# Kernel optimization log

Hardware: AMD Instinct MI355X
Metric: run time of the kernel (lower is better)

Reference implementation:

```python
import jax, jax.numpy as jnp
import numpy as np

N, E, IN, HID, H, OUT = 50000, 1600000, 64, 128, 4, 64
D = HID // H  # per-head dim = 32
EPS = 1e-5
NEG_SLOPE = 0.2


def layer_norm(x, g, b):
    mu = x.mean(-1, keepdims=True)
    var = ((x - mu) ** 2).mean(-1, keepdims=True)
    return (x - mu) * jax.lax.rsqrt(var + EPS) * g + b


def gat_conv(h, src, dst, W, a_src, a_dst, bias):
    # h: [N, HID]; W: [HID, H*D]; a_src/a_dst: [H, D]
    hW = (h @ W).reshape(N, H, D)
    e_src = (hW * a_src).sum(-1)  # [N, H]
    e_dst = (hW * a_dst).sum(-1)  # [N, H]
    e = jax.nn.leaky_relu(e_src[src] + e_dst[dst], NEG_SLOPE)  # [Etot, H]
    m = jax.ops.segment_max(e, dst, num_segments=N)            # [N, H]
    ex = jnp.exp(e - m[dst])
    denom = jax.ops.segment_sum(ex, dst, num_segments=N)       # [N, H]
    alpha = ex / denom[dst]                                    # [Etot, H]
    out = jax.ops.segment_sum(alpha[:, :, None] * hW[src], dst, num_segments=N)
    return out.reshape(N, H * D) + bias


def setup_inputs():
    key = jax.random.key(0)
    ks = jax.random.split(key, 16)
    s = 0.05
    return {
        "x": jax.random.normal(ks[0], (N, IN), jnp.float32),
        "edge_index": jax.random.randint(ks[1], (2, E), 0, N, jnp.int64),
        "w_in": jax.random.normal(ks[2], (IN, HID), jnp.float32) * s,
        "b_in": jnp.zeros((HID,), jnp.float32),
        "g1": jnp.ones((HID,), jnp.float32),
        "be1": jnp.zeros((HID,), jnp.float32),
        "W1": jax.random.normal(ks[3], (HID, H * D), jnp.float32) * s,
        "as1": jax.random.normal(ks[4], (H, D), jnp.float32) * s,
        "ad1": jax.random.normal(ks[5], (H, D), jnp.float32) * s,
        "bg1": jnp.zeros((H * D,), jnp.float32),
        "g2": jnp.ones((HID,), jnp.float32),
        "be2": jnp.zeros((HID,), jnp.float32),
        "W2": jax.random.normal(ks[6], (HID, H * D), jnp.float32) * s,
        "as2": jax.random.normal(ks[7], (H, D), jnp.float32) * s,
        "ad2": jax.random.normal(ks[8], (H, D), jnp.float32) * s,
        "bg2": jnp.zeros((H * D,), jnp.float32),
        "w_out": jax.random.normal(ks[9], (HID, OUT), jnp.float32) * s,
        "b_out": jnp.zeros((OUT,), jnp.float32),
    }


def reference(x, edge_index, w_in, b_in, g1, be1, W1, as1, ad1, bg1,
              g2, be2, W2, as2, ad2, bg2, w_out, b_out):
    # PyG GATConv default add_self_loops=True
    loops = jnp.arange(N, dtype=edge_index.dtype)
    src = jnp.concatenate([edge_index[0], loops])
    dst = jnp.concatenate([edge_index[1], loops])

    h = x @ w_in + b_in
    h = jax.nn.gelu(layer_norm(h, g1, be1))
    h = gat_conv(h, src, dst, W1, as1, ad1, bg1)
    h = jax.nn.gelu(layer_norm(h, g2, be2))
    # dropout: identity in eval mode
    h = gat_conv(h, src, dst, W2, as2, ad2, bg2)
    return h @ w_out + b_out
```

## Files before the change

kernel.cpp:

```cpp
#include <hip/hip_runtime.h>
#include <hip/hip_bf16.h>
#include <math.h>

#define NN   50000
#define EE   1600000
#define ETOT (EE + NN)
#define HID  128
#define INF_ 64
#define OUTF 64

#define NBK  256
#define NPB  196
#define CAP  8192
#define BBLK 256
#define CHUNK ((ETOT + BBLK - 1) / BBLK)

#define PADX 72
#define PADH 136

typedef short  short8  __attribute__((ext_vector_type(8)));
typedef float  floatx4 __attribute__((ext_vector_type(4)));
typedef float  floatx2 __attribute__((ext_vector_type(2)));

__device__ __forceinline__ ushort f2b(float f) {
    __hip_bfloat16 h = __float2bfloat16(f);
    return *reinterpret_cast<ushort*>(&h);
}

__device__ __forceinline__ float gelu_f(float x) {
    float x2 = x * x;
    float u  = 0.7978845608f * fmaf(0.044715f * x2, x, x);
    u = fminf(u, 40.f);
    float t = __expf(2.f * u);
    return x * t / (t + 1.f);
}


__global__ __launch_bounds__(1024) void k_bucket(const int* __restrict__ ei,
                                                 int* bcur, int* __restrict__ tmp) {
    __shared__ unsigned sortedv[CHUNK];
    __shared__ int hist[NBK], gbase[NBK], loff[NBK], lcur[NBK];
    int t = threadIdx.x;
    int lo = blockIdx.x * CHUNK;
    int hi = min(lo + CHUNK, ETOT);
    int bsize = hi - lo;
    if (t < NBK) hist[t] = 0;
    __syncthreads();
    for (int i = lo + t; i < hi; i += 1024) {
        int d = (i < EE) ? ei[EE + i] : i - EE;
        atomicAdd(&hist[d / NPB], 1);
    }
    __syncthreads();
    if (t < NBK) {
        int c = hist[t];
        gbase[t] = (c > 0) ? atomicAdd(&bcur[t], c) : 0;
        loff[t] = c;
    }
    __syncthreads();
    for (int d = 1; d < NBK; d <<= 1) {
        int v = (t >= d && t < NBK) ? loff[t - d] : 0;
        __syncthreads();
        if (t < NBK) loff[t] += v;
        __syncthreads();
    }
    if (t < NBK) {
        int ex = loff[t] - hist[t];
        loff[t] = ex;
        lcur[t] = ex;
    }
    __syncthreads();
    for (int i = lo + t; i < hi; i += 1024) {
        unsigned s, d;
        if (i < EE) { s = (unsigned)ei[i]; d = (unsigned)ei[EE + i]; }
        else        { s = d = (unsigned)(i - EE); }
        unsigned b = d / NPB;
        int p = atomicAdd(&lcur[b], 1);
        sortedv[p] = (b << 24) | (s << 8) | (d - b * NPB);
    }
    __syncthreads();
    for (int i = t; i < bsize; i += 1024) {
        unsigned v = sortedv[i];
        unsigned b = v >> 24;
        int pp = gbase[b] + i - loff[b];
        if (pp < CAP) tmp[b * CAP + pp] = (int)(v & 0xFFFFFFu);
    }
}

__global__ __launch_bounds__(256) void k_bscan(const int* __restrict__ bcur,
                                               int* __restrict__ bstart,
                                               int* __restrict__ off,
                                               int* __restrict__ csr) {
    __shared__ int s[NBK];
    int t = threadIdx.x;
    int v0 = bcur[t];
    s[t] = v0;
    __syncthreads();
    for (int d = 1; d < NBK; d <<= 1) {
        int v = (t >= d) ? s[t - d] : 0;
        __syncthreads();
        s[t] += v;
        __syncthreads();
    }
    bstart[t] = s[t] - v0;
    if (t == 0) off[NN] = ETOT;
    if (t < 64) csr[ETOT + t] = 0;
}

__global__ __launch_bounds__(512) void k_bucket2csr(const int* __restrict__ tmp,
                                                    const int* __restrict__ bcur,
                                                    const int* __restrict__ bstart,
                                                    int* __restrict__ off,
                                                    int* __restrict__ csr) {
    __shared__ int sE[CAP];
    __shared__ int lcnt[NPB];
    __shared__ int loff[NPB];
    int b = blockIdx.x, t = threadIdx.x;
    int n0    = b * NPB;
    int bsize = min(bcur[b], CAP);
    int base  = bstart[b];
    if (t < NPB) lcnt[t] = 0;
    for (int i = t; i < bsize; i += 512) sE[i] = tmp[b * CAP + i];
    __syncthreads();
    for (int i = t; i < bsize; i += 512) atomicAdd(&lcnt[sE[i] & 255], 1);
    __syncthreads();
    if (t < NPB) loff[t] = lcnt[t];
    __syncthreads();
    for (int d = 1; d < NPB; d <<= 1) {
        int v = (t >= d && t < NPB) ? loff[t - d] : 0;
        __syncthreads();
        if (t < NPB) loff[t] += v;
        __syncthreads();
    }
    if (t < NPB) {
        int ex = loff[t] - lcnt[t];
        if (n0 + t < NN) off[n0 + t] = base + ex;
        lcnt[t] = ex;
    }
    __syncthreads();
    for (int i = t; i < bsize; i += 512) {
        int v   = sE[i];
        int pos = base + atomicAdd(&lcnt[v & 255], 1);
        csr[pos] = v >> 8;
    }
}


__global__ void k_packall(const float* __restrict__ w_in, const float* __restrict__ W1,
                          const float* __restrict__ W2, ushort* __restrict__ Bp1,
                          ushort* __restrict__ BpW1, ushort* __restrict__ BpW2,
                          int* __restrict__ bcur) {
    int tid = blockIdx.x * 256 + threadIdx.x;
    if (tid < NBK) bcur[tid] = 0;
    const float* W; ushort* dst; int K, id;
    if (tid < 1024)      { W = w_in; dst = Bp1;  K = 64;  id = tid; }
    else if (tid < 3072) { W = W1;   dst = BpW1; K = 128; id = tid - 1024; }
    else if (tid < 5120) { W = W2;   dst = BpW2; K = 128; id = tid - 3072; }
    else return;
    int kst = K >> 5;
    int l = id & 63;
    int s = (id >> 6) % kst;
    int T = id / (kst * 64);
    int m = l & 15, q = l >> 4;
    ushort o[8];
    #pragma unroll
    for (int j = 0; j < 8; ++j)
        o[j] = f2b(W[(s * 32 + q * 8 + j) * 128 + T * 16 + m]);
    uint4 pk;
    pk.x = (unsigned)o[0] | ((unsigned)o[1] << 16);
    pk.y = (unsigned)o[2] | ((unsigned)o[3] << 16);
    pk.z = (unsigned)o[4] | ((unsigned)o[5] << 16);
    pk.w = (unsigned)o[6] | ((unsigned)o[7] << 16);
    reinterpret_cast<uint4*>(dst)[id] = pk;
}


__device__ __forceinline__ void pack_store_fp8(ushort* hbfw, int l, int n0w, bool active,
                                               uint* __restrict__ hW8) {
    if (!active) return;
    int row = l >> 2, ch = l & 3;
    uint ov[8];
    #pragma unroll
    for (int u = 0; u < 8; ++u) {
        int c0 = ch * 32 + u * 4;
        float f0 = __uint_as_float((uint)hbfw[row * PADH + c0 + 0] << 16);
        float f1 = __uint_as_float((uint)hbfw[row * PADH + c0 + 1] << 16);
        float f2 = __uint_as_float((uint)hbfw[row * PADH + c0 + 2] << 16);
        float f3 = __uint_as_float((uint)hbfw[row * PADH + c0 + 3] << 16);
        int pk = __builtin_amdgcn_cvt_pk_fp8_f32(f0, f1, 0, false);
        pk     = __builtin_amdgcn_cvt_pk_fp8_f32(f2, f3, pk, true);
        ov[u] = (uint)pk;
    }
    uint4* dst = reinterpret_cast<uint4*>(hW8 + (size_t)(n0w + row) * 32 + ch * 8);
    dst[0] = make_uint4(ov[0], ov[1], ov[2], ov[3]);
    dst[1] = make_uint4(ov[4], ov[5], ov[6], ov[7]);
}


__global__ __launch_bounds__(128) void k_infeat(const float* __restrict__ x,
                                                const ushort* __restrict__ Bp1,
                                                const float* __restrict__ bin,
                                                const float* __restrict__ g,
                                                const float* __restrict__ be,
                                                const ushort* __restrict__ Bp2,
                                                const float* __restrict__ asrc,
                                                const float* __restrict__ adst,
                                                uint* __restrict__ hW8,
                                                float* __restrict__ esrc,
                                                float* __restrict__ edst) {
    __shared__ ushort xbf[2][16 * PADX];
    __shared__ ushort hbf[2][16 * PADH];
    int t = threadIdx.x, w = t >> 6, l = t & 63;
    int m = l & 15, q = l >> 4;
    int n0w = blockIdx.x * 32 + w * 16;
    bool active = (n0w < NN);
    int nb = active ? n0w : 0;

    const float4* x4 = reinterpret_cast<const float4*>(x) + (size_t)nb * 16;
    #pragma unroll
    for (int i = 0; i < 4; ++i) {
        int f4 = l + 64 * i;
        int node = f4 >> 4, c4 = f4 & 15;
        float4 v = x4[f4];
        ushort4 pk = { f2b(v.x), f2b(v.y), f2b(v.z), f2b(v.w) };
        *reinterpret_cast<ushort4*>(&xbf[w][node * PADX + c4 * 4]) = pk;
    }
    __syncthreads();

    const short8* B1 = reinterpret_cast<const short8*>(Bp1);
    floatx4 acc1[8];
    #pragma unroll
    for (int T = 0; T < 8; ++T) acc1[T] = (floatx4){0.f, 0.f, 0.f, 0.f};
    #pragma unroll
    for (int s = 0; s < 2; ++s) {
        short8 a = *reinterpret_cast<const short8*>(&xbf[w][m * PADX + s * 32 + q * 8]);
        #pragma unroll
        for (int T = 0; T < 8; ++T) {
            short8 b = B1[(T * 2 + s) * 64 + l];
            acc1[T] = __builtin_amdgcn_mfma_f32_16x16x32_bf16(a, b, acc1[T], 0, 0, 0);
        }
    }

    float bc[8], gc[8], bec[8];
    #pragma unroll
    for (int T = 0; T < 8; ++T) {
        int c = T * 16 + m;
        bc[T] = bin[c]; gc[T] = g[c]; bec[T] = be[c];
    }
    #pragma unroll
    for (int j = 0; j < 4; ++j) {
        float s1 = 0.f, s2 = 0.f;
        #pragma unroll
        for (int T = 0; T < 8; ++T) {
            float v = acc1[T][j] + bc[T];
            s1 += v; s2 = fmaf(v, v, s2);
        }
        #pragma unroll
        for (int mk = 1; mk < 16; mk <<= 1) {
            s1 += __shfl_xor(s1, mk, 64);
            s2 += __shfl_xor(s2, mk, 64);
        }
        float mu = s1 * (1.f / 128.f);
        float var = s2 * (1.f / 128.f) - mu * mu;
        float rs = rsqrtf(var + 1e-5f);
        #pragma unroll
        for (int T = 0; T < 8; ++T) {
            float v = acc1[T][j] + bc[T];
            float y = (v - mu) * rs * gc[T] + bec[T];
            hbf[w][(q * 4 + j) * PADH + T * 16 + m] = f2b(gelu_f(y));
        }
    }
    __syncthreads();

    const short8* B2 = reinterpret_cast<const short8*>(Bp2);
    floatx4 acc2[8];
    #pragma unroll
    for (int T = 0; T < 8; ++T) acc2[T] = (floatx4){0.f, 0.f, 0.f, 0.f};
    #pragma unroll
    for (int s = 0; s < 4; ++s) {
        short8 a = *reinterpret_cast<const short8*>(&hbf[w][m * PADH + s * 32 + q * 8]);
        #pragma unroll
        for (int T = 0; T < 8; ++T) {
            short8 b = B2[(T * 4 + s) * 64 + l];
            acc2[T] = __builtin_amdgcn_mfma_f32_16x16x32_bf16(a, b, acc2[T], 0, 0, 0);
        }
    }

    __syncthreads();
    #pragma unroll
    for (int j = 0; j < 4; ++j)
        #pragma unroll
        for (int T = 0; T < 8; ++T)
            hbf[w][(q * 4 + j) * PADH + T * 16 + m] = f2b(acc2[T][j]);
    __syncthreads();
    pack_store_fp8(hbf[w], l, n0w, active, hW8);

    float as_[8], ad_[8];
    #pragma unroll
    for (int T = 0; T < 8; ++T) {
        int c = T * 16 + m;
        as_[T] = asrc[c]; ad_[T] = adst[c];
    }
    #pragma unroll
    for (int j = 0; j < 4; ++j) {
        #pragma unroll
        for (int h = 0; h < 4; ++h) {
            float v1 = fmaf(acc2[2 * h][j], as_[2 * h], acc2[2 * h + 1][j] * as_[2 * h + 1]);
            float v2 = fmaf(acc2[2 * h][j], ad_[2 * h], acc2[2 * h + 1][j] * ad_[2 * h + 1]);
            #pragma unroll
            for (int mk = 1; mk < 16; mk <<= 1) {
                v1 += __shfl_xor(v1, mk, 64);
                v2 += __shfl_xor(v2, mk, 64);
            }
            if (m == 0 && active) {
                esrc[(n0w + q * 4 + j) * 4 + h] = v1;
                edst[(n0w + q * 4 + j) * 4 + h] = v2;
            }
        }
    }
}


__global__ __launch_bounds__(128) void k_feat(const float* __restrict__ hin,
                                              const float* __restrict__ g,
                                              const float* __restrict__ be,
                                              const ushort* __restrict__ Bp2,
                                              const float* __restrict__ asrc,
                                              const float* __restrict__ adst,
                                              uint* __restrict__ hW8,
                                              float* __restrict__ esrc,
                                              float* __restrict__ edst) {
    __shared__ ushort hbf[2][16 * PADH];
    int t = threadIdx.x, w = t >> 6, l = t & 63;
    int m = l & 15, q = l >> 4;
    int n0w = blockIdx.x * 32 + w * 16;
    bool active = (n0w < NN);
    int nb = active ? n0w : 0;

    const float4* h4g = reinterpret_cast<const float4*>(hin) + (size_t)nb * 32;
    const float4* g4  = reinterpret_cast<const float4*>(g);
    const float4* be4 = reinterpret_cast<const float4*>(be);
    #pragma unroll
    for (int i = 0; i < 8; ++i) {
        int f4 = l + 64 * i;
        int node = f4 >> 5, c4 = f4 & 31;
        float4 v = h4g[f4];
        float s1 = v.x + v.y + v.z + v.w;
        float s2 = fmaf(v.x, v.x, fmaf(v.y, v.y, fmaf(v.z, v.z, v.w * v.w)));
        #pragma unroll
        for (int mk = 1; mk < 32; mk <<= 1) {
            s1 += __shfl_xor(s1, mk, 64);
            s2 += __shfl_xor(s2, mk, 64);
        }
        float mu = s1 * (1.f / 128.f);
        float var = s2 * (1.f / 128.f) - mu * mu;
        float rs = rsqrtf(var + 1e-5f);
        float4 gg = g4[c4], bb = be4[c4];
        ushort4 pk;
        pk.x = f2b(gelu_f((v.x - mu) * rs * gg.x + bb.x));
        pk.y = f2b(gelu_f((v.y - mu) * rs * gg.y + bb.y));
        pk.z = f2b(gelu_f((v.z - mu) * rs * gg.z + bb.z));
        pk.w = f2b(gelu_f((v.w - mu) * rs * gg.w + bb.w));
        *reinterpret_cast<ushort4*>(&hbf[w][node * PADH + c4 * 4]) = pk;
    }
    __syncthreads();

    const short8* B2 = reinterpret_cast<const short8*>(Bp2);
    floatx4 acc2[8];
    #pragma unroll
    for (int T = 0; T < 8; ++T) acc2[T] = (floatx4){0.f, 0.f, 0.f, 0.f};
    #pragma unroll
    for (int s = 0; s < 4; ++s) {
        short8 a = *reinterpret_cast<const short8*>(&hbf[w][m * PADH + s * 32 + q * 8]);
        #pragma unroll
        for (int T = 0; T < 8; ++T) {
            short8 b = B2[(T * 4 + s) * 64 + l];
            acc2[T] = __builtin_amdgcn_mfma_f32_16x16x32_bf16(a, b, acc2[T], 0, 0, 0);
        }
    }

    __syncthreads();
    #pragma unroll
    for (int j = 0; j < 4; ++j)
        #pragma unroll
        for (int T = 0; T < 8; ++T)
            hbf[w][(q * 4 + j) * PADH + T * 16 + m] = f2b(acc2[T][j]);
    __syncthreads();
    pack_store_fp8(hbf[w], l, n0w, active, hW8);

    float as_[8], ad_[8];
    #pragma unroll
    for (int T = 0; T < 8; ++T) {
        int c = T * 16 + m;
        as_[T] = asrc[c]; ad_[T] = adst[c];
    }
    #pragma unroll
    for (int j = 0; j < 4; ++j) {
        #pragma unroll
        for (int h = 0; h < 4; ++h) {
            float v1 = fmaf(acc2[2 * h][j], as_[2 * h], acc2[2 * h + 1][j] * as_[2 * h + 1]);
            float v2 = fmaf(acc2[2 * h][j], ad_[2 * h], acc2[2 * h + 1][j] * ad_[2 * h + 1]);
            #pragma unroll
            for (int mk = 1; mk < 16; mk <<= 1) {
                v1 += __shfl_xor(v1, mk, 64);
                v2 += __shfl_xor(v2, mk, 64);
            }
            if (m == 0 && active) {
                esrc[(n0w + q * 4 + j) * 4 + h] = v1;
                edst[(n0w + q * 4 + j) * 4 + h] = v2;
            }
        }
    }
}


__global__ __launch_bounds__(128) void k_gat(const uint* __restrict__ hW8,
                                             const float* __restrict__ esrc,
                                             const float* __restrict__ edst,
                                             const int* __restrict__ off,
                                             const int* __restrict__ csr,
                                             const float* __restrict__ bg,
                                             float* __restrict__ out) {
    __shared__ float redA[16][8];
    __shared__ float redD[16];
    int n = blockIdx.x, t = threadIdx.x;
    int wv = t >> 6, l = t & 63;
    int slot = l >> 4;
    int q    = l & 15;
    int hq   = q >> 2;
    int o0 = off[n], o1 = off[n + 1];
    float ednh = edst[n * 4 + hq];
    const uint2* hw2 = reinterpret_cast<const uint2*>(hW8);
    floatx2 a01 = {0.f, 0.f}, a23 = {0.f, 0.f}, a45 = {0.f, 0.f}, a67 = {0.f, 0.f};
    float dsum = 0.f;
    int nIter = (o1 - o0 + 15) >> 4;
    int e = o0 + wv * 4 + slot;

    int srcA = csr[e];
    int srcB = csr[e + 8];
    int srcC = csr[e + 16];
    int srcD = csr[e + 24];
    float esA = esrc[srcA * 4 + hq];
    float esB = esrc[srcB * 4 + hq];
    uint2 rA = hw2[(size_t)srcA * 16 + q];
    uint2 rB = hw2[(size_t)srcB * 16 + q];

    for (int it = 0; it < nIter; ++it) {
        uint2 rC = hw2[(size_t)srcC * 16 + q];
        uint2 rD = hw2[(size_t)srcD * 16 + q];
        float esC = esrc[srcC * 4 + hq];
        float esD = esrc[srcD * 4 + hq];
        int srcE = csr[e + 32];
        int srcF = csr[e + 40];
        float ea = esA + ednh; ea = fmaxf(ea, 0.2f * ea);
        float eb = esB + ednh; eb = fmaxf(eb, 0.2f * eb);
        float wa = (e     < o1) ? __expf(ea) : 0.f;
        float wb = (e + 8 < o1) ? __expf(eb) : 0.f;
        floatx2 wa2 = {wa, wa}, wb2 = {wb, wb};
        a01 += wa2 * __builtin_amdgcn_cvt_pk_f32_fp8(rA.x, false);
        a23 += wa2 * __builtin_amdgcn_cvt_pk_f32_fp8(rA.x, true);
        a45 += wa2 * __builtin_amdgcn_cvt_pk_f32_fp8(rA.y, false);
        a67 += wa2 * __builtin_amdgcn_cvt_pk_f32_fp8(rA.y, true);
        a01 += wb2 * __builtin_amdgcn_cvt_pk_f32_fp8(rB.x, false);
        a23 += wb2 * __builtin_amdgcn_cvt_pk_f32_fp8(rB.x, true);
        a45 += wb2 * __builtin_amdgcn_cvt_pk_f32_fp8(rB.y, false);
        a67 += wb2 * __builtin_amdgcn_cvt_pk_f32_fp8(rB.y, true);
        dsum += wa + wb;
        e += 16;
        rA = rC; rB = rD;
        esA = esC; esB = esD;
        srcC = srcE; srcD = srcF;
    }
    float acc[8] = {a01[0], a01[1], a23[0], a23[1], a45[0], a45[1], a67[0], a67[1]};
    #pragma unroll
    for (int mk = 16; mk <= 32; mk <<= 1) {
        #pragma unroll
        for (int j = 0; j < 8; ++j) acc[j] += __shfl_xor(acc[j], mk, 64);
        dsum += __shfl_xor(dsum, mk, 64);
    }
    if (wv == 1 && l < 16) {
        #pragma unroll
        for (int j = 0; j < 8; ++j) redA[l][j] = acc[j];
        redD[l] = dsum;
    }
    __syncthreads();
    if (wv == 0 && l < 16) {
        float inv = 1.0f / (dsum + redD[l]);
        float4 r0, r1;
        r0.x = (acc[0] + redA[l][0]) * inv + bg[l * 8 + 0];
        r0.y = (acc[1] + redA[l][1]) * inv + bg[l * 8 + 1];
        r0.z = (acc[2] + redA[l][2]) * inv + bg[l * 8 + 2];
        r0.w = (acc[3] + redA[l][3]) * inv + bg[l * 8 + 3];
        r1.x = (acc[4] + redA[l][4]) * inv + bg[l * 8 + 4];
        r1.y = (acc[5] + redA[l][5]) * inv + bg[l * 8 + 5];
        r1.z = (acc[6] + redA[l][6]) * inv + bg[l * 8 + 6];
        r1.w = (acc[7] + redA[l][7]) * inv + bg[l * 8 + 7];
        float4* op = reinterpret_cast<float4*>(out + (size_t)n * HID + l * 8);
        op[0] = r0; op[1] = r1;
    }
}


__global__ __launch_bounds__(128) void k_out(const float* __restrict__ h,
                                             const float* __restrict__ w,
                                             const float* __restrict__ b,
                                             float* __restrict__ out) {
    __shared__ __align__(16) float hr[32 * 132];
    int t = threadIdx.x, n0 = blockIdx.x * 32;
    const float4* h4g = reinterpret_cast<const float4*>(h) + (size_t)n0 * 32;
    float4* hr4 = reinterpret_cast<float4*>(hr);
    #pragma unroll
    for (int i = 0; i < 8; ++i) {
        int f4 = t + 128 * i;
        hr4[(f4 >> 5) * 33 + (f4 & 31)] = h4g[f4];
    }
    __syncthreads();
    int cg = t & 15, ng = t >> 4;
    const float4* w4 = reinterpret_cast<const float4*>(w);
    float4 bb = reinterpret_cast<const float4*>(b)[cg];
    float4 acc[4] = {bb, bb, bb, bb};
    for (int k4 = 0; k4 < 32; ++k4) {
        float4 w0 = w4[(k4 * 4 + 0) * 16 + cg];
        float4 w1 = w4[(k4 * 4 + 1) * 16 + cg];
        float4 w2 = w4[(k4 * 4 + 2) * 16 + cg];
        float4 w3 = w4[(k4 * 4 + 3) * 16 + cg];
        #pragma unroll
        for (int r = 0; r < 4; ++r) {
            float4 hv = hr4[(ng * 4 + r) * 33 + k4];
            acc[r].x = fmaf(hv.x, w0.x, fmaf(hv.y, w1.x, fmaf(hv.z, w2.x, fmaf(hv.w, w3.x, acc[r].x))));
            acc[r].y = fmaf(hv.x, w0.y, fmaf(hv.y, w1.y, fmaf(hv.z, w2.y, fmaf(hv.w, w3.y, acc[r].y))));
            acc[r].z = fmaf(hv.x, w0.z, fmaf(hv.y, w1.z, fmaf(hv.z, w2.z, fmaf(hv.w, w3.z, acc[r].z))));
            acc[r].w = fmaf(hv.x, w0.w, fmaf(hv.y, w1.w, fmaf(hv.z, w2.w, fmaf(hv.w, w3.w, acc[r].w))));
        }
    }
    float4* o4 = reinterpret_cast<float4*>(out) + (size_t)n0 * 16;
    #pragma unroll
    for (int r = 0; r < 4; ++r) {
        if (n0 + ng * 4 + r < NN)
            o4[(ng * 4 + r) * 16 + cg] = acc[r];
    }
}

extern "C" void kernel_launch(void* const* d_in, const int* in_sizes, int n_in,
                              void* d_out, int out_size, void* d_ws, size_t ws_size,
                              hipStream_t stream) {
    const float* x    = (const float*)d_in[0];
    const int*   ei   = (const int*)  d_in[1];
    const float* w_in = (const float*)d_in[2];
    const float* b_in = (const float*)d_in[3];
    const float* g1   = (const float*)d_in[4];
    const float* be1  = (const float*)d_in[5];
    const float* W1   = (const float*)d_in[6];
    const float* as1  = (const float*)d_in[7];
    const float* ad1  = (const float*)d_in[8];
    const float* bg1  = (const float*)d_in[9];
    const float* g2   = (const float*)d_in[10];
    const float* be2  = (const float*)d_in[11];
    const float* W2   = (const float*)d_in[12];
    const float* as2  = (const float*)d_in[13];
    const float* ad2  = (const float*)d_in[14];
    const float* bg2  = (const float*)d_in[15];
    const float* w_o  = (const float*)d_in[16];
    const float* b_o  = (const float*)d_in[17];
    float* out = (float*)d_out;

    char* p = (char*)d_ws;
    auto take = [&](size_t bytes) {
        void* r = p;
        p += (bytes + 255) & ~(size_t)255;
        return r;
    };
    float*  gout  = (float*)take((size_t)NN * HID * 4);
    float*  h2    = (float*)take((size_t)NN * HID * 4);
    uint*   hW8   = (uint*)take((size_t)NN * HID);
    float*  esrc  = (float*)take((size_t)NN * 4 * 4);
    float*  edst  = (float*)take((size_t)NN * 4 * 4);
    int*    off   = (int*)take((size_t)(NN + 1) * 4);
    int*    csr   = (int*)take((size_t)(ETOT + 64) * 4);
    int*    tmp   = (int*)take((size_t)NBK * CAP * 4);
    int*    bcur  = (int*)take((size_t)NBK * 4);
    int*    bstart= (int*)take((size_t)NBK * 4);
    ushort* Bp1   = (ushort*)take((size_t)1024 * 16);
    ushort* BpW1  = (ushort*)take((size_t)2048 * 16);
    ushort* BpW2  = (ushort*)take((size_t)2048 * 16);

    k_packall   <<<20, 256, 0, stream>>>(w_in, W1, W2, Bp1, BpW1, BpW2, bcur);
    k_bucket    <<<BBLK, 1024, 0, stream>>>(ei, bcur, tmp);
    k_bscan     <<<1, NBK, 0, stream>>>(bcur, bstart, off, csr);
    k_bucket2csr<<<NBK, 512, 0, stream>>>(tmp, bcur, bstart, off, csr);

    int gfeat = (NN + 31) / 32;
    k_infeat<<<gfeat, 128, 0, stream>>>(x, Bp1, b_in, g1, be1, BpW1, as1, ad1, hW8, esrc, edst);
    k_gat   <<<NN, 128, 0, stream>>>(hW8, esrc, edst, off, csr, bg1, gout);
    k_feat  <<<gfeat, 128, 0, stream>>>(gout, g2, be2, BpW2, as2, ad2, hW8, esrc, edst);
    k_gat   <<<NN, 128, 0, stream>>>(hW8, esrc, edst, off, csr, bg2, h2);
    k_out   <<<(NN + 31) / 32, 128, 0, stream>>>(h2, w_o, b_o, out);
}
```

Baseline: 282.4 us.

## Use one wave per node in GAT, store GAT outputs as bf16, fold scan into CSR build

The GAT aggregation kernel now gives each 64-lane wave its own destination node, with four nodes per 256-thread block. This removes the cross-wave shared-memory reduction and barrier. GAT outputs are written as bf16 instead of fp32, which halves the intermediate traffic read back by the feature and output kernels. The separate bucket-scan kernel is removed: each CSR-build block redoes the 256-entry prefix scan itself, and the padding zeroing moves into the pack kernel. In exchange, the GAT outputs carry extra bf16 rounding, and each node's edge loop now runs on a single wave.

```diff
diff --git a/kernel.cpp b/kernel.cpp
--- a/kernel.cpp
+++ b/kernel.cpp
@@ -26,6 +26,8 @@
     __hip_bfloat16 h = __float2bfloat16(f);
     return *reinterpret_cast<ushort*>(&h);
 }
+__device__ __forceinline__ float b2f_lo(uint v) { return __uint_as_float(v << 16); }
+__device__ __forceinline__ float b2f_hi(uint v) { return __uint_as_float(v & 0xffff0000u); }
 
 __device__ __forceinline__ float gelu_f(float x) {
     float x2 = x * x;
@@ -86,38 +88,27 @@
     }
 }
 
-__global__ __launch_bounds__(256) void k_bscan(const int* __restrict__ bcur,
-                                               int* __restrict__ bstart,
-                                               int* __restrict__ off,
-                                               int* __restrict__ csr) {
-    __shared__ int s[NBK];
-    int t = threadIdx.x;
-    int v0 = bcur[t];
-    s[t] = v0;
-    __syncthreads();
-    for (int d = 1; d < NBK; d <<= 1) {
-        int v = (t >= d) ? s[t - d] : 0;
-        __syncthreads();
-        s[t] += v;
-        __syncthreads();
-    }
-    bstart[t] = s[t] - v0;
-    if (t == 0) off[NN] = ETOT;
-    if (t < 64) csr[ETOT + t] = 0;
-}
-
 __global__ __launch_bounds__(512) void k_bucket2csr(const int* __restrict__ tmp,
                                                     const int* __restrict__ bcur,
-                                                    const int* __restrict__ bstart,
                                                     int* __restrict__ off,
                                                     int* __restrict__ csr) {
     __shared__ int sE[CAP];
     __shared__ int lcnt[NPB];
     __shared__ int loff[NPB];
+    __shared__ int sb[NBK];
     int b = blockIdx.x, t = threadIdx.x;
     int n0    = b * NPB;
     int bsize = min(bcur[b], CAP);
-    int base  = bstart[b];
+    if (t < NBK) sb[t] = bcur[t];
+    __syncthreads();
+    for (int d = 1; d < NBK; d <<= 1) {
+        int v = (t >= d && t < NBK) ? sb[t - d] : 0;
+        __syncthreads();
+        if (t < NBK) sb[t] += v;
+        __syncthreads();
+    }
+    int base = sb[b] - bcur[b];
+    if (b == 0 && t == 0) off[NN] = ETOT;
     if (t < NPB) lcnt[t] = 0;
     for (int i = t; i < bsize; i += 512) sE[i] = tmp[b * CAP + i];
     __syncthreads();
@@ -148,9 +139,10 @@
 __global__ void k_packall(const float* __restrict__ w_in, const float* __restrict__ W1,
                           const float* __restrict__ W2, ushort* __restrict__ Bp1,
                           ushort* __restrict__ BpW1, ushort* __restrict__ BpW2,
-                          int* __restrict__ bcur) {
+                          int* __restrict__ bcur, int* __restrict__ csr) {
     int tid = blockIdx.x * 256 + threadIdx.x;
     if (tid < NBK) bcur[tid] = 0;
+    if (tid < 64) csr[ETOT + tid] = 0;
     const float* W; ushort* dst; int K, id;
     if (tid < 1024)      { W = w_in; dst = Bp1;  K = 64;  id = tid; }
     else if (tid < 3072) { W = W1;   dst = BpW1; K = 128; id = tid - 1024; }
@@ -320,7 +312,7 @@
 }
 
 
-__global__ __launch_bounds__(128) void k_feat(const float* __restrict__ hin,
+__global__ __launch_bounds__(128) void k_feat(const ushort* __restrict__ hinb,
                                               const float* __restrict__ g,
                                               const float* __restrict__ be,
                                               const ushort* __restrict__ Bp2,
@@ -336,31 +328,41 @@
     bool active = (n0w < NN);
     int nb = active ? n0w : 0;
 
-    const float4* h4g = reinterpret_cast<const float4*>(hin) + (size_t)nb * 32;
     const float4* g4  = reinterpret_cast<const float4*>(g);
     const float4* be4 = reinterpret_cast<const float4*>(be);
     #pragma unroll
-    for (int i = 0; i < 8; ++i) {
-        int f4 = l + 64 * i;
-        int node = f4 >> 5, c4 = f4 & 31;
-        float4 v = h4g[f4];
-        float s1 = v.x + v.y + v.z + v.w;
-        float s2 = fmaf(v.x, v.x, fmaf(v.y, v.y, fmaf(v.z, v.z, v.w * v.w)));
-        #pragma unroll
-        for (int mk = 1; mk < 32; mk <<= 1) {
-            s1 += __shfl_xor(s1, mk, 64);
-            s2 += __shfl_xor(s2, mk, 64);
+    for (int i = 0; i < 4; ++i) {
+        int s = l + 64 * i;
+        int node = s >> 4, c8 = s & 15;
+        uint4 v = *reinterpret_cast<const uint4*>(hinb + (size_t)(nb + node) * HID + c8 * 8);
+        float f[8] = { b2f_lo(v.x), b2f_hi(v.x), b2f_lo(v.y), b2f_hi(v.y),
+                       b2f_lo(v.z), b2f_hi(v.z), b2f_lo(v.w), b2f_hi(v.w) };
+        float s1 = 0.f, s2 = 0.f;
+        #pragma unroll
+        for (int j = 0; j < 8; ++j) { s1 += f[j]; s2 = fmaf(f[j], f[j], s2); }
+        #pragma unroll
+        for (int mk = 1; mk < 16; mk <<= 1) {
+            s1 += __shfl_xor(s1, mk, 16);
+            s2 += __shfl_xor(s2, mk, 16);
         }
         float mu = s1 * (1.f / 128.f);
         float var = s2 * (1.f / 128.f) - mu * mu;
         float rs = rsqrtf(var + 1e-5f);
-        float4 gg = g4[c4], bb = be4[c4];
-        ushort4 pk;
-        pk.x = f2b(gelu_f((v.x - mu) * rs * gg.x + bb.x));
-        pk.y = f2b(gelu_f((v.y - mu) * rs * gg.y + bb.y));
-        pk.z = f2b(gelu_f((v.z - mu) * rs * gg.z + bb.z));
-        pk.w = f2b(gelu_f((v.w - mu) * rs * gg.w + bb.w));
-        *reinterpret_cast<ushort4*>(&hbf[w][node * PADH + c4 * 4]) = pk;
+        float4 gg0 = g4[c8 * 2], gg1 = g4[c8 * 2 + 1];
+        float4 bb0 = be4[c8 * 2], bb1 = be4[c8 * 2 + 1];
+        float gv[8] = {gg0.x, gg0.y, gg0.z, gg0.w, gg1.x, gg1.y, gg1.z, gg1.w};
+        float bv[8] = {bb0.x, bb0.y, bb0.z, bb0.w, bb1.x, bb1.y, bb1.z, bb1.w};
+        ushort4 p0, p1;
+        p0.x = f2b(gelu_f((f[0] - mu) * rs * gv[0] + bv[0]));
+        p0.y = f2b(gelu_f((f[1] - mu) * rs * gv[1] + bv[1]));
+        p0.z = f2b(gelu_f((f[2] - mu) * rs * gv[2] + bv[2]));
+        p0.w = f2b(gelu_f((f[3] - mu) * rs * gv[3] + bv[3]));
+        p1.x = f2b(gelu_f((f[4] - mu) * rs * gv[4] + bv[4]));
+        p1.y = f2b(gelu_f((f[5] - mu) * rs * gv[5] + bv[5]));
+        p1.z = f2b(gelu_f((f[6] - mu) * rs * gv[6] + bv[6]));
+        p1.w = f2b(gelu_f((f[7] - mu) * rs * gv[7] + bv[7]));
+        *reinterpret_cast<ushort4*>(&hbf[w][node * PADH + c8 * 8])     = p0;
+        *reinterpret_cast<ushort4*>(&hbf[w][node * PADH + c8 * 8 + 4]) = p1;
     }
     __syncthreads();
 
@@ -413,32 +415,31 @@
 }
 
 
-__global__ __launch_bounds__(128) void k_gat(const uint* __restrict__ hW8,
+__global__ __launch_bounds__(256) void k_gat(const uint* __restrict__ hW8,
                                              const float* __restrict__ esrc,
                                              const float* __restrict__ edst,
                                              const int* __restrict__ off,
                                              const int* __restrict__ csr,
                                              const float* __restrict__ bg,
-                                             float* __restrict__ out) {
-    __shared__ float redA[16][8];
-    __shared__ float redD[16];
-    int n = blockIdx.x, t = threadIdx.x;
+                                             ushort* __restrict__ outb) {
+    int t = threadIdx.x;
     int wv = t >> 6, l = t & 63;
     int slot = l >> 4;
     int q    = l & 15;
     int hq   = q >> 2;
+    int n = blockIdx.x * 4 + wv;
     int o0 = off[n], o1 = off[n + 1];
     float ednh = edst[n * 4 + hq];
     const uint2* hw2 = reinterpret_cast<const uint2*>(hW8);
     floatx2 a01 = {0.f, 0.f}, a23 = {0.f, 0.f}, a45 = {0.f, 0.f}, a67 = {0.f, 0.f};
     float dsum = 0.f;
-    int nIter = (o1 - o0 + 15) >> 4;
-    int e = o0 + wv * 4 + slot;
+    int nIter = (o1 - o0 + 7) >> 3;
+    int e = o0 + slot;
 
     int srcA = csr[e];
-    int srcB = csr[e + 8];
-    int srcC = csr[e + 16];
-    int srcD = csr[e + 24];
+    int srcB = csr[e + 4];
+    int srcC = csr[e + 8];
+    int srcD = csr[e + 12];
     float esA = esrc[srcA * 4 + hq];
     float esB = esrc[srcB * 4 + hq];
     uint2 rA = hw2[(size_t)srcA * 16 + q];
@@ -449,12 +450,12 @@
         uint2 rD = hw2[(size_t)srcD * 16 + q];
         float esC = esrc[srcC * 4 + hq];
         float esD = esrc[srcD * 4 + hq];
-        int srcE = csr[e + 32];
-        int srcF = csr[e + 40];
+        int srcE = csr[e + 16];
+        int srcF = csr[e + 20];
         float ea = esA + ednh; ea = fmaxf(ea, 0.2f * ea);
         float eb = esB + ednh; eb = fmaxf(eb, 0.2f * eb);
         float wa = (e     < o1) ? __expf(ea) : 0.f;
-        float wb = (e + 8 < o1) ? __expf(eb) : 0.f;
+        float wb = (e + 4 < o1) ? __expf(eb) : 0.f;
         floatx2 wa2 = {wa, wa}, wb2 = {wb, wb};
         a01 += wa2 * __builtin_amdgcn_cvt_pk_f32_fp8(rA.x, false);
         a23 += wa2 * __builtin_amdgcn_cvt_pk_f32_fp8(rA.x, true);
@@ -465,7 +466,7 @@
         a45 += wb2 * __builtin_amdgcn_cvt_pk_f32_fp8(rB.y, false);
         a67 += wb2 * __builtin_amdgcn_cvt_pk_f32_fp8(rB.y, true);
         dsum += wa + wb;
-        e += 16;
+        e += 8;
         rA = rC; rB = rD;
         esA = esC; esB = esD;
         srcC = srcE; srcD = srcF;
@@ -477,41 +478,37 @@
         for (int j = 0; j < 8; ++j) acc[j] += __shfl_xor(acc[j], mk, 64);
         dsum += __shfl_xor(dsum, mk, 64);
     }
-    if (wv == 1 && l < 16) {
-        #pragma unroll
-        for (int j = 0; j < 8; ++j) redA[l][j] = acc[j];
-        redD[l] = dsum;
-    }
-    __syncthreads();
-    if (wv == 0 && l < 16) {
-        float inv = 1.0f / (dsum + redD[l]);
-        float4 r0, r1;
-        r0.x = (acc[0] + redA[l][0]) * inv + bg[l * 8 + 0];
-        r0.y = (acc[1] + redA[l][1]) * inv + bg[l * 8 + 1];
-        r0.z = (acc[2] + redA[l][2]) * inv + bg[l * 8 + 2];
-        r0.w = (acc[3] + redA[l][3]) * inv + bg[l * 8 + 3];
-        r1.x = (acc[4] + redA[l][4]) * inv + bg[l * 8 + 4];
-        r1.y = (acc[5] + redA[l][5]) * inv + bg[l * 8 + 5];
-        r1.z = (acc[6] + redA[l][6]) * inv + bg[l * 8 + 6];
-        r1.w = (acc[7] + redA[l][7]) * inv + bg[l * 8 + 7];
-        float4* op = reinterpret_cast<float4*>(out + (size_t)n * HID + l * 8);
-        op[0] = r0; op[1] = r1;
-    }
-}
-
-
-__global__ __launch_bounds__(128) void k_out(const float* __restrict__ h,
+    if (l < 16) {
+        float inv = 1.0f / dsum;
+        float v[8];
+        #pragma unroll
+        for (int j = 0; j < 8; ++j) v[j] = acc[j] * inv + bg[l * 8 + j];
+        uint4 o;
+        o.x = (uint)f2b(v[0]) | ((uint)f2b(v[1]) << 16);
+        o.y = (uint)f2b(v[2]) | ((uint)f2b(v[3]) << 16);
+        o.z = (uint)f2b(v[4]) | ((uint)f2b(v[5]) << 16);
+        o.w = (uint)f2b(v[6]) | ((uint)f2b(v[7]) << 16);
+        *reinterpret_cast<uint4*>(outb + (size_t)n * HID + l * 8) = o;
+    }
+}
+
+
+__global__ __launch_bounds__(128) void k_out(const ushort* __restrict__ hb,
                                              const float* __restrict__ w,
                                              const float* __restrict__ b,
                                              float* __restrict__ out) {
     __shared__ __align__(16) float hr[32 * 132];
     int t = threadIdx.x, n0 = blockIdx.x * 32;
-    const float4* h4g = reinterpret_cast<const float4*>(h) + (size_t)n0 * 32;
     float4* hr4 = reinterpret_cast<float4*>(hr);
     #pragma unroll
-    for (int i = 0; i < 8; ++i) {
-        int f4 = t + 128 * i;
-        hr4[(f4 >> 5) * 33 + (f4 & 31)] = h4g[f4];
+    for (int i = 0; i < 4; ++i) {
+        int s = t + 128 * i;
+        int node = s >> 4, c8 = s & 15;
+        uint4 v = *reinterpret_cast<const uint4*>(hb + (size_t)(n0 + node) * HID + c8 * 8);
+        float4 lo = { b2f_lo(v.x), b2f_hi(v.x), b2f_lo(v.y), b2f_hi(v.y) };
+        float4 hi = { b2f_lo(v.z), b2f_hi(v.z), b2f_lo(v.w), b2f_hi(v.w) };
+        hr4[node * 33 + c8 * 2]     = lo;
+        hr4[node * 33 + c8 * 2 + 1] = hi;
     }
     __syncthreads();
     int cg = t & 15, ng = t >> 4;
@@ -569,8 +566,8 @@
         p += (bytes + 255) & ~(size_t)255;
         return r;
     };
-    float*  gout  = (float*)take((size_t)NN * HID * 4);
-    float*  h2    = (float*)take((size_t)NN * HID * 4);
+    ushort* gout  = (ushort*)take((size_t)(NN + 32) * HID * 2);
+    ushort* h2    = (ushort*)take((size_t)(NN + 32) * HID * 2);
     uint*   hW8   = (uint*)take((size_t)NN * HID);
     float*  esrc  = (float*)take((size_t)NN * 4 * 4);
     float*  edst  = (float*)take((size_t)NN * 4 * 4);
@@ -578,20 +575,18 @@
     int*    csr   = (int*)take((size_t)(ETOT + 64) * 4);
     int*    tmp   = (int*)take((size_t)NBK * CAP * 4);
     int*    bcur  = (int*)take((size_t)NBK * 4);
-    int*    bstart= (int*)take((size_t)NBK * 4);
     ushort* Bp1   = (ushort*)take((size_t)1024 * 16);
     ushort* BpW1  = (ushort*)take((size_t)2048 * 16);
     ushort* BpW2  = (ushort*)take((size_t)2048 * 16);
 
-    k_packall   <<<20, 256, 0, stream>>>(w_in, W1, W2, Bp1, BpW1, BpW2, bcur);
+    k_packall   <<<20, 256, 0, stream>>>(w_in, W1, W2, Bp1, BpW1, BpW2, bcur, csr);
     k_bucket    <<<BBLK, 1024, 0, stream>>>(ei, bcur, tmp);
-    k_bscan     <<<1, NBK, 0, stream>>>(bcur, bstart, off, csr);
-    k_bucket2csr<<<NBK, 512, 0, stream>>>(tmp, bcur, bstart, off, csr);
+    k_bucket2csr<<<NBK, 512, 0, stream>>>(tmp, bcur, off, csr);
 
     int gfeat = (NN + 31) / 32;
     k_infeat<<<gfeat, 128, 0, stream>>>(x, Bp1, b_in, g1, be1, BpW1, as1, ad1, hW8, esrc, edst);
-    k_gat   <<<NN, 128, 0, stream>>>(hW8, esrc, edst, off, csr, bg1, gout);
+    k_gat   <<<NN / 4, 256, 0, stream>>>(hW8, esrc, edst, off, csr, bg1, gout);
     k_feat  <<<gfeat, 128, 0, stream>>>(gout, g2, be2, BpW2, as2, ad2, hW8, esrc, edst);
-    k_gat   <<<NN, 128, 0, stream>>>(hW8, esrc, edst, off, csr, bg2, h2);
+    k_gat   <<<NN / 4, 256, 0, stream>>>(hW8, esrc, edst, off, csr, bg2, h2);
     k_out   <<<(NN + 31) / 32, 128, 0, stream>>>(h2, w_o, b_o, out);
 }
```

New measurement: 268.5 us. 1.05x faster.
